# Kernel tuning notes

Measured on AMD Instinct MI355X. Metric: run time of the kernel, lower is better.

Reference implementation:

```python
import jax, jax.numpy as jnp
import numpy as np

N_NODES = 50000
BN_EPS = 1e-5


def setup_inputs() -> dict:
    key = jax.random.key(0)
    ks = jax.random.split(key, 16)
    N, IN, H, OUT, E = N_NODES, 512, 128, 64, 800000
    s = lambda fi, fo: 1.0 / np.sqrt(fi)
    inp = {
        'x': jax.random.normal(ks[0], (N, IN), dtype=jnp.float32),
        'edge_index': jax.random.randint(ks[1], (2, E), 0, N, dtype=jnp.int32),
        # mlpA: Linear(N -> H)
        'WA': jax.random.uniform(ks[2], (H, N), jnp.float32, -s(N, H), s(N, H)),
        'bA': jax.random.uniform(ks[3], (H,), jnp.float32, -s(N, H), s(N, H)),
        # mlpX: Linear(IN -> H)
        'WX': jax.random.uniform(ks[4], (H, IN), jnp.float32, -s(IN, H), s(IN, H)),
        'bX': jax.random.uniform(ks[5], (H,), jnp.float32, -s(IN, H), s(IN, H)),
        # W: Linear(2H -> H)
        'W': jax.random.uniform(ks[6], (H, 2 * H), jnp.float32, -s(2 * H, H), s(2 * H, H)),
        'bW': jax.random.uniform(ks[7], (H,), jnp.float32, -s(2 * H, H), s(2 * H, H)),
        # mlp_final layer 1: Linear(H -> H) + BN
        'Wf1': jax.random.uniform(ks[8], (H, H), jnp.float32, -s(H, H), s(H, H)),
        'bf1': jax.random.uniform(ks[9], (H,), jnp.float32, -s(H, H), s(H, H)),
        'gamma': jnp.ones((H,), jnp.float32),
        'beta': jnp.zeros((H,), jnp.float32),
        # mlp_final layer 2: Linear(H -> OUT)
        'Wf2': jax.random.uniform(ks[10], (OUT, H), jnp.float32, -s(H, OUT), s(H, OUT)),
        'bf2': jax.random.uniform(ks[11], (OUT,), jnp.float32, -s(H, OUT), s(H, OUT)),
    }
    return inp


def _batchnorm(x, gamma, beta):
    # training-mode BN over the node/batch axis (biased variance, as in torch)
    mean = jnp.mean(x, axis=0)
    var = jnp.var(x, axis=0)
    return (x - mean) * jax.lax.rsqrt(var + BN_EPS) * gamma + beta


def reference(x, edge_index, WA, bA, WX, bX, W, bW, Wf1, bf1, gamma, beta, Wf2, bf2):
    row, col = edge_index[0], edge_index[1]
    row = row - row.min()
    # xA = A @ WA.T + bA  where A[i,j]=1 per (row,col) edge (duplicates sum).
    # Equivalent SpMM: gather columns of WA at `col`, segment-sum into `row`.
    xA = jax.ops.segment_sum(WA.T[col], row, num_segments=N_NODES) + bA  # [N, H]
    xX = x @ WX.T + bX  # [N, H]
    h = jnp.concatenate([xA, xX], axis=-1) @ W.T + bW  # [N, H]
    h = jax.nn.relu(h + xA + xX)
    # mlp_final (num_layers=2): Linear -> ReLU -> BN -> (dropout off) -> Linear
    h = jax.nn.relu(h @ Wf1.T + bf1)
    h = _batchnorm(h, gamma, beta)
    out = h @ Wf2.T + bf2  # [N, OUT]
    return out
```

## Files before the change

### kernel.cpp

```cpp
#include <hip/hip_runtime.h>

typedef __bf16 bf16_t;
typedef __bf16 bf16x8 __attribute__((ext_vector_type(8)));
typedef float f32x4 __attribute__((ext_vector_type(4)));

#define IN_DIM 512
#define H_DIM 128
#define OUT_DIM 64
#define BN_EPS 1e-5f
#define SCAN_BLK 2048

#define MFMA(a, b, c) __builtin_amdgcn_mfma_f32_16x16x32_bf16(a, b, c, 0, 0, 0)

__device__ __forceinline__ float ld_adapt(const void* p, size_t i, int isbf) {
    return isbf ? (float)((const bf16_t*)p)[i] : ((const float*)p)[i];
}

__device__ __forceinline__ void split8(const float* p, bf16x8& hi, bf16x8& lo) {
    f32x4 v0 = *(const f32x4*)p;
    f32x4 v1 = *(const f32x4*)(p + 4);
#pragma unroll
    for (int i = 0; i < 8; ++i) {
        float f = (i < 4) ? v0[i] : v1[i - 4];
        bf16_t h = (bf16_t)f;
        hi[i] = h;
        lo[i] = (bf16_t)(f - (float)h);
    }
}

__global__ void k_init(const void* bA, const void* bX, const void* bW, const void* bf1,
                       const void* gamma, const void* beta, const void* bf2,
                       float* __restrict__ dst, int* __restrict__ flag) {
    __shared__ int s_isbf;
    if (threadIdx.x == 0) {
        unsigned u = *(const unsigned*)gamma;
        int f = (u == 0x3F803F80u) ? 1 : 0;
        *flag = f;
        s_isbf = f;
    }
    __syncthreads();
    int isbf = s_isbf;
    int t = threadIdx.x;
    dst[t] = ld_adapt(bA, t, isbf);
    dst[128 + t] = ld_adapt(bX, t, isbf);
    dst[256 + t] = ld_adapt(bW, t, isbf);
    dst[384 + t] = ld_adapt(bf1, t, isbf);
    dst[512 + t] = ld_adapt(gamma, t, isbf);
    dst[640 + t] = ld_adapt(beta, t, isbf);
    if (t < OUT_DIM) dst[768 + t] = ld_adapt(bf2, t, isbf);
}

__global__ __launch_bounds__(256) void k_transpose(const void* __restrict__ WA,
                                                   float* __restrict__ WAT, int N,
                                                   const int* __restrict__ flag) {
    __shared__ float t[64][130];
    int isbf = *flag;
    int n0 = blockIdx.x * 64;
    int tid = threadIdx.x;
#pragma unroll
    for (int i = 0; i < 32; ++i) {
        int lin = i * 256 + tid;
        int h = lin >> 6, nl = lin & 63;
        int n = n0 + nl;
        t[nl][h] = (n < N) ? ld_adapt(WA, (size_t)h * N + n, isbf) : 0.f;
    }
    __syncthreads();
#pragma unroll
    for (int i = 0; i < 32; ++i) {
        int lin = i * 256 + tid;
        int nl = lin >> 7, h = lin & 127;
        int n = n0 + nl;
        if (n < N) WAT[(size_t)n * H_DIM + h] = t[nl][h];
    }
}

__global__ __launch_bounds__(256) void k_prep(const int* __restrict__ rows, int E,
                                              int* __restrict__ bmin, int* __restrict__ cnt) {
    __shared__ int sm[4];
    int i = blockIdx.x * 256 + threadIdx.x;
    int m = 0x7fffffff;
    if (i < E) {
        int r = rows[i];
        m = r;
        atomicAdd(&cnt[r], 1);
    }
    for (int off = 32; off; off >>= 1) m = min(m, __shfl_xor(m, off, 64));
    if ((threadIdx.x & 63) == 0) sm[threadIdx.x >> 6] = m;
    __syncthreads();
    if (threadIdx.x == 0)
        bmin[blockIdx.x] = min(min(sm[0], sm[1]), min(sm[2], sm[3]));
}

__global__ __launch_bounds__(256) void k_scan1(const int* __restrict__ cnt,
                                               int* __restrict__ offs,
                                               int* __restrict__ bsum, int N) {
    __shared__ int ts[256];
    int base = blockIdx.x * SCAN_BLK;
    int t = threadIdx.x;
    int v[8], s = 0;
#pragma unroll
    for (int i = 0; i < 8; ++i) {
        int idx = base + t * 8 + i;
        v[i] = (idx < N) ? cnt[idx] : 0;
        s += v[i];
    }
    ts[t] = s;
    __syncthreads();
    for (int off = 1; off < 256; off <<= 1) {
        int x = (t >= off) ? ts[t - off] : 0;
        __syncthreads();
        ts[t] += x;
        __syncthreads();
    }
    int run = ts[t] - s;
#pragma unroll
    for (int i = 0; i < 8; ++i) {
        int idx = base + t * 8 + i;
        if (idx < N) offs[idx] = run;
        run += v[i];
    }
    if (t == 255) bsum[blockIdx.x] = ts[255];
}

__global__ __launch_bounds__(256) void k_scan2(int* __restrict__ bsum, int* __restrict__ offs,
                                               int NB, int N, const int* __restrict__ bmin,
                                               int nbmin, int* __restrict__ minbuf) {
    __shared__ int sm[256];
    int t = threadIdx.x;
    int m = 0x7fffffff;
    for (int i = t; i < nbmin; i += 256) m = min(m, bmin[i]);
    sm[t] = m;
    __syncthreads();
    for (int off = 128; off; off >>= 1) {
        if (t < off) sm[t] = min(sm[t], sm[t + off]);
        __syncthreads();
    }
    if (t == 0) {
        *minbuf = sm[0];
        int run = 0;
        for (int b = 0; b < NB; ++b) {
            int v = bsum[b];
            bsum[b] = run;
            run += v;
        }
        offs[N] = run;
    }
}

__global__ __launch_bounds__(256) void k_scan3(int* __restrict__ offs, const int* __restrict__ bsum,
                                               int* __restrict__ cursor, int N) {
    int i = blockIdx.x * 256 + threadIdx.x;
    if (i >= N) return;
    int v = offs[i] + bsum[i / SCAN_BLK];
    offs[i] = v;
    cursor[i] = v;
}

__global__ __launch_bounds__(256) void k_build(const int* __restrict__ rows,
                                               const int* __restrict__ cols, int E,
                                               int* __restrict__ cursor,
                                               int* __restrict__ scol) {
    int i = blockIdx.x * 256 + threadIdx.x;
    if (i >= E) return;
    int r = rows[i];
    int pos = atomicAdd(&cursor[r], 1);
    scol[pos] = cols[i];
}

__global__ __launch_bounds__(256) void k_gather(const int* __restrict__ offs,
                                                const int* __restrict__ scol,
                                                const float* __restrict__ WAT,
                                                const float* __restrict__ bA_f,
                                                const int* __restrict__ minbuf,
                                                float* __restrict__ xA, int N) {
    int wave = threadIdx.x >> 6, lane = threadIdx.x & 63;
    int r = blockIdx.x * 4 + wave;
    if (r >= N) return;
    int b = r + *minbuf;
    int s = 0, e = 0;
    if (b < N) {
        s = offs[b];
        e = offs[b + 1];
    }
    float2 a0 = {0.f, 0.f}, a1 = {0.f, 0.f};
    int i = s;
    for (; i + 3 < e; i += 4) {
        int c0 = scol[i], c1 = scol[i + 1], c2 = scol[i + 2], c3 = scol[i + 3];
        float2 w0 = *(const float2*)(WAT + (size_t)c0 * H_DIM + lane * 2);
        float2 w1 = *(const float2*)(WAT + (size_t)c1 * H_DIM + lane * 2);
        float2 w2 = *(const float2*)(WAT + (size_t)c2 * H_DIM + lane * 2);
        float2 w3 = *(const float2*)(WAT + (size_t)c3 * H_DIM + lane * 2);
        a0.x += w0.x + w2.x; a0.y += w0.y + w2.y;
        a1.x += w1.x + w3.x; a1.y += w1.y + w3.y;
    }
    for (; i < e; ++i) {
        int c = scol[i];
        float2 w = *(const float2*)(WAT + (size_t)c * H_DIM + lane * 2);
        a0.x += w.x; a0.y += w.y;
    }
    float2 bias = *(const float2*)(bA_f + lane * 2);
    float2 out = {a0.x + a1.x + bias.x, a0.y + a1.y + bias.y};
    *(float2*)(xA + (size_t)r * H_DIM + lane * 2) = out;
}

__device__ __forceinline__ void pack_frag(const void* __restrict__ W, bf16_t* __restrict__ hi,
                                          bf16_t* __restrict__ lo, int K, int NC,
                                          int addres, int isbf, int f, int lane) {
    int ks = f / (NC >> 4), nt = f % (NC >> 4);
    int n = nt * 16 + (lane & 15);
    int k0 = ks * 32 + (lane >> 4) * 8;
    bf16_t* dh = hi + (size_t)f * 512 + lane * 8;
    bf16_t* dl = lo + (size_t)f * 512 + lane * 8;
#pragma unroll
    for (int j = 0; j < 8; ++j) {
        int kk = k0 + j;
        float v = ld_adapt(W, (size_t)n * K + kk, isbf);
        if (addres && (kk == n || kk == n + H_DIM)) v += 1.f;
        bf16_t h = (bf16_t)v;
        dh[j] = h;
        dl[j] = (bf16_t)(v - (float)h);
    }
}

__global__ __launch_bounds__(256) void k_pack3(const void* WX, bf16_t* WXh, bf16_t* WXl,
                                               const void* W, bf16_t* Wh, bf16_t* Wl,
                                               const void* Wf1, bf16_t* Wf1h, bf16_t* Wf1l,
                                               const int* __restrict__ flag) {
    int g = blockIdx.x * 256 + threadIdx.x;
    int f = g >> 6, lane = g & 63;
    int isbf = *flag;
    if (f < 128)
        pack_frag(WX, WXh, WXl, IN_DIM, H_DIM, 0, isbf, f, lane);
    else if (f < 192)
        pack_frag(W, Wh, Wl, 2 * H_DIM, H_DIM, 1, isbf, f - 128, lane);
    else if (f < 224)
        pack_frag(Wf1, Wf1h, Wf1l, H_DIM, H_DIM, 0, isbf, f - 192, lane);
}

__global__ __launch_bounds__(512) void k_fuseA(
    const void* __restrict__ x, const float* __restrict__ xAf,
    const bf16_t* __restrict__ WXh, const bf16_t* __restrict__ WXl,
    const bf16_t* __restrict__ Wh, const bf16_t* __restrict__ Wl,
    const bf16_t* __restrict__ Wf1h, const bf16_t* __restrict__ Wf1l,
    const float* __restrict__ smallf, float* __restrict__ h2,
    double* __restrict__ sums, double* __restrict__ sumsq,
    const int* __restrict__ flag, int M) {
    __shared__ float ax[64 * 132];
    __shared__ float ls_sum[H_DIM], ls_sq[H_DIM];
    int tid = threadIdx.x;
    int wave = tid >> 6, lane = tid & 63, l16 = lane & 15, quad = lane >> 4;
    int band = wave & 3, half = wave >> 2;
    int ntb = half * 4;
    int mbase = blockIdx.x * 64 + band * 16;
    int isbf = *flag;
    int r0 = min(mbase + l16, M - 1);
    const float* bX = smallf + 128;
    const float* bW = smallf + 256;
    const float* bf1 = smallf + 384;

    if (tid < H_DIM) {
        ls_sum[tid] = 0.f;
        ls_sq[tid] = 0.f;
    }

    bf16x8 zero8;
#pragma unroll
    for (int i = 0; i < 8; ++i) zero8[i] = (bf16_t)0.f;

    f32x4 acc[4];
#pragma unroll
    for (int nt = 0; nt < 4; ++nt) acc[nt] = f32x4{0.f, 0.f, 0.f, 0.f};
    {
        size_t offx = (size_t)r0 * IN_DIM + quad * 8;
        for (int ks = 0; ks < 16; ++ks) {
            bf16x8 ah, al;
            if (isbf) {
                ah = *(const bf16x8*)((const bf16_t*)x + offx + ks * 32);
                al = zero8;
            } else {
                split8((const float*)x + offx + ks * 32, ah, al);
            }
            const bf16_t* bhp = WXh + ((size_t)ks * 8 + ntb) * 512 + lane * 8;
            const bf16_t* blp = WXl + ((size_t)ks * 8 + ntb) * 512 + lane * 8;
#pragma unroll
            for (int nt = 0; nt < 4; ++nt) {
                bf16x8 bh = *(const bf16x8*)(bhp + nt * 512);
                bf16x8 bl = *(const bf16x8*)(blp + nt * 512);
                acc[nt] = MFMA(ah, bh, acc[nt]);
                acc[nt] = MFMA(ah, bl, acc[nt]);
                acc[nt] = MFMA(al, bh, acc[nt]);
            }
        }
    }
#pragma unroll
    for (int nt = 0; nt < 4; ++nt) {
        int col = (ntb + nt) * 16 + l16;
        float b = bX[col];
#pragma unroll
        for (int r = 0; r < 4; ++r) {
            int lr = band * 16 + quad * 4 + r;
            ax[lr * 132 + col] = acc[nt][r] + b;
        }
    }
    __syncthreads();

#pragma unroll
    for (int nt = 0; nt < 4; ++nt) acc[nt] = f32x4{0.f, 0.f, 0.f, 0.f};
    for (int ks = 0; ks < 8; ++ks) {
        bf16x8 ah, al;
        if (ks < 4)
            split8(xAf + (size_t)r0 * H_DIM + ks * 32 + quad * 8, ah, al);
        else
            split8(ax + (band * 16 + l16) * 132 + (ks - 4) * 32 + quad * 8, ah, al);
        const bf16_t* bhp = Wh + ((size_t)ks * 8 + ntb) * 512 + lane * 8;
        const bf16_t* blp = Wl + ((size_t)ks * 8 + ntb) * 512 + lane * 8;
#pragma unroll
        for (int nt = 0; nt < 4; ++nt) {
            bf16x8 bh = *(const bf16x8*)(bhp + nt * 512);
            bf16x8 bl = *(const bf16x8*)(blp + nt * 512);
            acc[nt] = MFMA(ah, bh, acc[nt]);
            acc[nt] = MFMA(ah, bl, acc[nt]);
            acc[nt] = MFMA(al, bh, acc[nt]);
        }
    }
    __syncthreads();
#pragma unroll
    for (int nt = 0; nt < 4; ++nt) {
        int col = (ntb + nt) * 16 + l16;
        float b = bW[col];
#pragma unroll
        for (int r = 0; r < 4; ++r) {
            int lr = band * 16 + quad * 4 + r;
            ax[lr * 132 + col] = fmaxf(acc[nt][r] + b, 0.f);
        }
    }
    __syncthreads();

#pragma unroll
    for (int nt = 0; nt < 4; ++nt) acc[nt] = f32x4{0.f, 0.f, 0.f, 0.f};
    for (int ks = 0; ks < 4; ++ks) {
        bf16x8 ah, al;
        split8(ax + (band * 16 + l16) * 132 + ks * 32 + quad * 8, ah, al);
        const bf16_t* bhp = Wf1h + ((size_t)ks * 8 + ntb) * 512 + lane * 8;
        const bf16_t* blp = Wf1l + ((size_t)ks * 8 + ntb) * 512 + lane * 8;
#pragma unroll
        for (int nt = 0; nt < 4; ++nt) {
            bf16x8 bh = *(const bf16x8*)(bhp + nt * 512);
            bf16x8 bl = *(const bf16x8*)(blp + nt * 512);
            acc[nt] = MFMA(ah, bh, acc[nt]);
            acc[nt] = MFMA(ah, bl, acc[nt]);
            acc[nt] = MFMA(al, bh, acc[nt]);
        }
    }
#pragma unroll
    for (int nt = 0; nt < 4; ++nt) {
        int col = (ntb + nt) * 16 + l16;
        float b = bf1[col];
        float s = 0.f, s2 = 0.f;
#pragma unroll
        for (int r = 0; r < 4; ++r) {
            int row = mbase + quad * 4 + r;
            if (row < M) {
                float v = fmaxf(acc[nt][r] + b, 0.f);
                h2[(size_t)row * H_DIM + col] = v;
                s += v;
                s2 += v * v;
            }
        }
        s += __shfl_xor(s, 16, 64);
        s += __shfl_xor(s, 32, 64);
        s2 += __shfl_xor(s2, 16, 64);
        s2 += __shfl_xor(s2, 32, 64);
        if (quad == 0) {
            atomicAdd(&ls_sum[col], s);
            atomicAdd(&ls_sq[col], s2);
        }
    }
    __syncthreads();
    if (tid < H_DIM) {
        atomicAdd(&sums[tid], (double)ls_sum[tid]);
        atomicAdd(&sumsq[tid], (double)ls_sq[tid]);
    }
}

__global__ __launch_bounds__(256) void k_fuseB(
    const float* __restrict__ h2, const void* __restrict__ Wf2,
    const float* __restrict__ smallf, const double* __restrict__ sums,
    const double* __restrict__ sumsq, void* __restrict__ outv,
    const int* __restrict__ flag, int M) {
    __shared__ bf16_t wh[16 * 512];
    __shared__ bf16_t wl[16 * 512];
    __shared__ float aw[H_DIM], cw[H_DIM], b2[OUT_DIM];
    int t = threadIdx.x;
    int isbf = *flag;
    const float* gamma_f = smallf + 512;
    const float* beta_f = smallf + 640;
    const float* bf2_f = smallf + 768;

    if (t < H_DIM) {
        double mean = sums[t] / (double)M;
        double var = sumsq[t] / (double)M - mean * mean;
        if (var < 0) var = 0;
        float a = gamma_f[t] * rsqrtf((float)var + BN_EPS);
        aw[t] = a;
        cw[t] = beta_f[t] - (float)mean * a;
    }
    __syncthreads();
    if (t < OUT_DIM) {
        float acc = bf2_f[t];
        for (int j = 0; j < H_DIM; ++j) acc += ld_adapt(Wf2, (size_t)t * H_DIM + j, isbf) * cw[j];
        b2[t] = acc;
    }
    for (int u = t; u < 1024; u += 256) {
        int f = u >> 6, ln = u & 63;
        int ks = f >> 2, nt = f & 3;
        int n = nt * 16 + (ln & 15);
        int k0 = ks * 32 + (ln >> 4) * 8;
#pragma unroll
        for (int j = 0; j < 8; ++j) {
            float v = ld_adapt(Wf2, (size_t)n * H_DIM + k0 + j, isbf) * aw[k0 + j];
            bf16_t h = (bf16_t)v;
            wh[f * 512 + ln * 8 + j] = h;
            wl[f * 512 + ln * 8 + j] = (bf16_t)(v - (float)h);
        }
    }
    __syncthreads();

    int wave = t >> 6, lane = t & 63, l16 = lane & 15, quad = lane >> 4;
    int mbase = blockIdx.x * 64 + wave * 16;
    int r0 = min(mbase + l16, M - 1);
    f32x4 acc4[4];
#pragma unroll
    for (int nt = 0; nt < 4; ++nt) acc4[nt] = f32x4{0.f, 0.f, 0.f, 0.f};
    for (int ks = 0; ks < 4; ++ks) {
        bf16x8 ah, al;
        split8(h2 + (size_t)r0 * H_DIM + ks * 32 + quad * 8, ah, al);
#pragma unroll
        for (int nt = 0; nt < 4; ++nt) {
            bf16x8 bh = *(const bf16x8*)(wh + (ks * 4 + nt) * 512 + lane * 8);
            bf16x8 bl = *(const bf16x8*)(wl + (ks * 4 + nt) * 512 + lane * 8);
            acc4[nt] = MFMA(ah, bh, acc4[nt]);
            acc4[nt] = MFMA(ah, bl, acc4[nt]);
            acc4[nt] = MFMA(al, bh, acc4[nt]);
        }
    }
#pragma unroll
    for (int nt = 0; nt < 4; ++nt) {
        int col = nt * 16 + l16;
        float b = b2[col];
#pragma unroll
        for (int r = 0; r < 4; ++r) {
            int row = mbase + quad * 4 + r;
            if (row < M) {
                float v = acc4[nt][r] + b;
                if (isbf)
                    ((bf16_t*)outv)[(size_t)row * OUT_DIM + col] = (bf16_t)v;
                else
                    ((float*)outv)[(size_t)row * OUT_DIM + col] = v;
            }
        }
    }
}

extern "C" void kernel_launch(void* const* d_in, const int* in_sizes, int n_in,
                              void* d_out, int out_size, void* d_ws, size_t ws_size,
                              hipStream_t stream) {
    const void* x = d_in[0];
    const int* ei = (const int*)d_in[1];
    const void* WA = d_in[2];
    const void* bA = d_in[3];
    const void* WX = d_in[4];
    const void* bX = d_in[5];
    const void* W = d_in[6];
    const void* bW = d_in[7];
    const void* Wf1 = d_in[8];
    const void* bf1 = d_in[9];
    const void* gamma = d_in[10];
    const void* beta = d_in[11];
    const void* Wf2 = d_in[12];
    const void* bf2 = d_in[13];

    const int N = in_sizes[0] / IN_DIM;
    const int E = in_sizes[1] / 2;
    const int* rows = ei;
    const int* cols = ei + E;
    const int eblocks = (E + 255) / 256;

    char* ws = (char*)d_ws;
    size_t off = 0;
    auto alloc = [&](size_t bytes) {
        char* p = ws + off;
        off += (bytes + 255) & ~(size_t)255;
        return p;
    };
    int* flag = (int*)alloc(4);
    int* minbuf = (int*)alloc(4);
    float* smallf = (float*)alloc(832 * 4);
    double* sums = (double*)alloc(2 * H_DIM * 8);
    double* sumsq = sums + H_DIM;
    bf16_t* WXp_h = (bf16_t*)alloc((size_t)IN_DIM * H_DIM * 2);
    bf16_t* WXp_l = (bf16_t*)alloc((size_t)IN_DIM * H_DIM * 2);
    bf16_t* Wp_h = (bf16_t*)alloc((size_t)256 * H_DIM * 2);
    bf16_t* Wp_l = (bf16_t*)alloc((size_t)256 * H_DIM * 2);
    bf16_t* Wf1p_h = (bf16_t*)alloc((size_t)H_DIM * H_DIM * 2);
    bf16_t* Wf1p_l = (bf16_t*)alloc((size_t)H_DIM * H_DIM * 2);
    int* cnt = (int*)alloc((size_t)N * 4);
    int* offs = (int*)alloc(((size_t)N + 1) * 4);
    int* cursor = (int*)alloc((size_t)N * 4);
    int* bsum = (int*)alloc(64 * 4);
    int* bmin = (int*)alloc((size_t)eblocks * 4);
    int* scol = (int*)alloc((size_t)E * 4);
    float* WAT = (float*)alloc((size_t)N * H_DIM * 4);
    float* xAf = (float*)alloc((size_t)N * H_DIM * 4);
    float* h2 = WAT;

    float* bA_f = smallf + 0;

    hipMemsetAsync(cnt, 0, (size_t)N * 4, stream);
    hipMemsetAsync(sums, 0, 2 * H_DIM * 8, stream);

    k_init<<<1, 128, 0, stream>>>(bA, bX, bW, bf1, gamma, beta, bf2, smallf, flag);
    k_transpose<<<(N + 63) / 64, 256, 0, stream>>>(WA, WAT, N, flag);
    k_pack3<<<56, 256, 0, stream>>>(WX, WXp_h, WXp_l, W, Wp_h, Wp_l, Wf1, Wf1p_h, Wf1p_l, flag);

    k_prep<<<eblocks, 256, 0, stream>>>(rows, E, bmin, cnt);
    int NB = (N + SCAN_BLK - 1) / SCAN_BLK;
    k_scan1<<<NB, 256, 0, stream>>>(cnt, offs, bsum, N);
    k_scan2<<<1, 256, 0, stream>>>(bsum, offs, NB, N, bmin, eblocks, minbuf);
    k_scan3<<<(N + 255) / 256, 256, 0, stream>>>(offs, bsum, cursor, N);
    k_build<<<eblocks, 256, 0, stream>>>(rows, cols, E, cursor, scol);
    k_gather<<<(N + 3) / 4, 256, 0, stream>>>(offs, scol, WAT, bA_f, minbuf, xAf, N);

    int fblocks = (N + 63) / 64;
    k_fuseA<<<fblocks, 512, 0, stream>>>(x, xAf, WXp_h, WXp_l, Wp_h, Wp_l, Wf1p_h, Wf1p_l,
                                         smallf, h2, sums, sumsq, flag, N);
    k_fuseB<<<fblocks, 256, 0, stream>>>(h2, Wf2, smallf, sums, sumsq, d_out, flag, N);
}
```

Measured before the change: 487.7 us.

## Software-pipeline fused MLP loads, shrink blocks, and widen gather unroll

The fused MLP kernel now double-buffers its A and B operand loads from global memory, so the next k-step's data is fetched while the current MFMAs run. Blocks shrink from 64 rows and 512 threads to 32 rows and 256 threads, with launch bounds asking for two blocks per CU. The SpMM gather loop is unrolled to 8 loads with four accumulators to keep more memory requests in flight. The extra prefetch buffers raise register pressure, which could reduce occupancy.

Measured after the change: 503.5 us. 1.03x slower.

```diff
diff --git a/kernel.cpp b/kernel.cpp
--- a/kernel.cpp
+++ b/kernel.cpp
@@ -25,6 +25,34 @@
         bf16_t h = (bf16_t)f;
         hi[i] = h;
         lo[i] = (bf16_t)(f - (float)h);
+    }
+}
+
+__device__ __forceinline__ void loadAraw(const void* x, size_t elemoff, int isbf,
+                                         f32x4& p0, f32x4& p1) {
+    if (isbf) {
+        p0 = *(const f32x4*)((const bf16_t*)x + elemoff);
+    } else {
+        const float* fp = (const float*)x + elemoff;
+        p0 = *(const f32x4*)fp;
+        p1 = *(const f32x4*)(fp + 4);
+    }
+}
+
+__device__ __forceinline__ void cvtA(const f32x4& p0, const f32x4& p1, int isbf,
+                                     bf16x8& ah, bf16x8& al) {
+    if (isbf) {
+        ah = __builtin_bit_cast(bf16x8, p0);
+#pragma unroll
+        for (int i = 0; i < 8; ++i) al[i] = (bf16_t)0.f;
+    } else {
+#pragma unroll
+        for (int i = 0; i < 8; ++i) {
+            float f = (i < 4) ? p0[i] : p1[i - 4];
+            bf16_t h = (bf16_t)f;
+            ah[i] = h;
+            al[i] = (bf16_t)(f - (float)h);
+        }
     }
 }
 
@@ -182,24 +210,34 @@
         s = offs[b];
         e = offs[b + 1];
     }
-    float2 a0 = {0.f, 0.f}, a1 = {0.f, 0.f};
+    float2 a0 = {0.f, 0.f}, a1 = {0.f, 0.f}, a2 = {0.f, 0.f}, a3 = {0.f, 0.f};
     int i = s;
-    for (; i + 3 < e; i += 4) {
-        int c0 = scol[i], c1 = scol[i + 1], c2 = scol[i + 2], c3 = scol[i + 3];
+    for (; i + 7 < e; i += 8) {
+        float2 w[8];
+#pragma unroll
+        for (int j = 0; j < 8; ++j) {
+            int c = scol[i + j];
+            w[j] = *(const float2*)(WAT + (size_t)c * H_DIM + lane * 2);
+        }
+        a0.x += w[0].x + w[4].x; a0.y += w[0].y + w[4].y;
+        a1.x += w[1].x + w[5].x; a1.y += w[1].y + w[5].y;
+        a2.x += w[2].x + w[6].x; a2.y += w[2].y + w[6].y;
+        a3.x += w[3].x + w[7].x; a3.y += w[3].y + w[7].y;
+    }
+    for (; i + 1 < e; i += 2) {
+        int c0 = scol[i], c1 = scol[i + 1];
         float2 w0 = *(const float2*)(WAT + (size_t)c0 * H_DIM + lane * 2);
         float2 w1 = *(const float2*)(WAT + (size_t)c1 * H_DIM + lane * 2);
-        float2 w2 = *(const float2*)(WAT + (size_t)c2 * H_DIM + lane * 2);
-        float2 w3 = *(const float2*)(WAT + (size_t)c3 * H_DIM + lane * 2);
-        a0.x += w0.x + w2.x; a0.y += w0.y + w2.y;
-        a1.x += w1.x + w3.x; a1.y += w1.y + w3.y;
-    }
-    for (; i < e; ++i) {
+        a0.x += w0.x; a0.y += w0.y;
+        a1.x += w1.x; a1.y += w1.y;
+    }
+    if (i < e) {
         int c = scol[i];
         float2 w = *(const float2*)(WAT + (size_t)c * H_DIM + lane * 2);
-        a0.x += w.x; a0.y += w.y;
+        a2.x += w.x; a2.y += w.y;
     }
     float2 bias = *(const float2*)(bA_f + lane * 2);
-    float2 out = {a0.x + a1.x + bias.x, a0.y + a1.y + bias.y};
+    float2 out = {a0.x + a1.x + a2.x + a3.x + bias.x, a0.y + a1.y + a2.y + a3.y + bias.y};
     *(float2*)(xA + (size_t)r * H_DIM + lane * 2) = out;
 }
 
@@ -237,7 +275,7 @@
         pack_frag(Wf1, Wf1h, Wf1l, H_DIM, H_DIM, 0, isbf, f - 192, lane);
 }
 
-__global__ __launch_bounds__(512) void k_fuseA(
+__global__ __launch_bounds__(256, 2) void k_fuseA(
     const void* __restrict__ x, const float* __restrict__ xAf,
     const bf16_t* __restrict__ WXh, const bf16_t* __restrict__ WXl,
     const bf16_t* __restrict__ Wh, const bf16_t* __restrict__ Wl,
@@ -245,13 +283,13 @@
     const float* __restrict__ smallf, float* __restrict__ h2,
     double* __restrict__ sums, double* __restrict__ sumsq,
     const int* __restrict__ flag, int M) {
-    __shared__ float ax[64 * 132];
+    __shared__ float ax[32 * 132];
     __shared__ float ls_sum[H_DIM], ls_sq[H_DIM];
     int tid = threadIdx.x;
     int wave = tid >> 6, lane = tid & 63, l16 = lane & 15, quad = lane >> 4;
-    int band = wave & 3, half = wave >> 2;
+    int band = wave & 1, half = wave >> 1;
     int ntb = half * 4;
-    int mbase = blockIdx.x * 64 + band * 16;
+    int mbase = blockIdx.x * 32 + band * 16;
     int isbf = *flag;
     int r0 = min(mbase + l16, M - 1);
     const float* bX = smallf + 128;
@@ -263,32 +301,41 @@
         ls_sq[tid] = 0.f;
     }
 
-    bf16x8 zero8;
-#pragma unroll
-    for (int i = 0; i < 8; ++i) zero8[i] = (bf16_t)0.f;
+    auto loadB = [&](const bf16_t* __restrict__ H, const bf16_t* __restrict__ L, int fb,
+                     bf16x8 bh[4], bf16x8 bl[4]) {
+        const bf16_t* hp = H + (size_t)fb * 512 + lane * 8;
+        const bf16_t* lp = L + (size_t)fb * 512 + lane * 8;
+#pragma unroll
+        for (int nt = 0; nt < 4; ++nt) {
+            bh[nt] = *(const bf16x8*)(hp + nt * 512);
+            bl[nt] = *(const bf16x8*)(lp + nt * 512);
+        }
+    };
 
     f32x4 acc[4];
+    bf16x8 bh[2][4], bl[2][4];
+    f32x4 pa[2][2];
+
 #pragma unroll
     for (int nt = 0; nt < 4; ++nt) acc[nt] = f32x4{0.f, 0.f, 0.f, 0.f};
     {
         size_t offx = (size_t)r0 * IN_DIM + quad * 8;
+        loadAraw(x, offx, isbf, pa[0][0], pa[0][1]);
+        loadB(WXh, WXl, ntb, bh[0], bl[0]);
+#pragma unroll
         for (int ks = 0; ks < 16; ++ks) {
+            int cur = ks & 1, nxt = cur ^ 1;
+            if (ks < 15) {
+                loadAraw(x, offx + (ks + 1) * 32, isbf, pa[nxt][0], pa[nxt][1]);
+                loadB(WXh, WXl, (ks + 1) * 8 + ntb, bh[nxt], bl[nxt]);
+            }
             bf16x8 ah, al;
-            if (isbf) {
-                ah = *(const bf16x8*)((const bf16_t*)x + offx + ks * 32);
-                al = zero8;
-            } else {
-                split8((const float*)x + offx + ks * 32, ah, al);
-            }
-            const bf16_t* bhp = WXh + ((size_t)ks * 8 + ntb) * 512 + lane * 8;
-            const bf16_t* blp = WXl + ((size_t)ks * 8 + ntb) * 512 + lane * 8;
+            cvtA(pa[cur][0], pa[cur][1], isbf, ah, al);
 #pragma unroll
             for (int nt = 0; nt < 4; ++nt) {
-                bf16x8 bh = *(const bf16x8*)(bhp + nt * 512);
-                bf16x8 bl = *(const bf16x8*)(blp + nt * 512);
-                acc[nt] = MFMA(ah, bh, acc[nt]);
-                acc[nt] = MFMA(ah, bl, acc[nt]);
-                acc[nt] = MFMA(al, bh, acc[nt]);
+                acc[nt] = MFMA(ah, bh[cur][nt], acc[nt]);
+                acc[nt] = MFMA(ah, bl[cur][nt], acc[nt]);
+                acc[nt] = MFMA(al, bh[cur][nt], acc[nt]);
             }
         }
     }
@@ -306,21 +353,31 @@
 
 #pragma unroll
     for (int nt = 0; nt < 4; ++nt) acc[nt] = f32x4{0.f, 0.f, 0.f, 0.f};
-    for (int ks = 0; ks < 8; ++ks) {
-        bf16x8 ah, al;
-        if (ks < 4)
-            split8(xAf + (size_t)r0 * H_DIM + ks * 32 + quad * 8, ah, al);
-        else
-            split8(ax + (band * 16 + l16) * 132 + (ks - 4) * 32 + quad * 8, ah, al);
-        const bf16_t* bhp = Wh + ((size_t)ks * 8 + ntb) * 512 + lane * 8;
-        const bf16_t* blp = Wl + ((size_t)ks * 8 + ntb) * 512 + lane * 8;
-#pragma unroll
-        for (int nt = 0; nt < 4; ++nt) {
-            bf16x8 bh = *(const bf16x8*)(bhp + nt * 512);
-            bf16x8 bl = *(const bf16x8*)(blp + nt * 512);
-            acc[nt] = MFMA(ah, bh, acc[nt]);
-            acc[nt] = MFMA(ah, bl, acc[nt]);
-            acc[nt] = MFMA(al, bh, acc[nt]);
+    {
+        size_t aoff = (size_t)r0 * H_DIM + quad * 8;
+        const float* axp = ax + (band * 16 + l16) * 132 + quad * 8;
+        pa[0][0] = *(const f32x4*)(xAf + aoff);
+        pa[0][1] = *(const f32x4*)(xAf + aoff + 4);
+        loadB(Wh, Wl, ntb, bh[0], bl[0]);
+#pragma unroll
+        for (int ks = 0; ks < 8; ++ks) {
+            int cur = ks & 1, nxt = cur ^ 1;
+            if (ks < 7) loadB(Wh, Wl, (ks + 1) * 8 + ntb, bh[nxt], bl[nxt]);
+            if (ks < 3) {
+                pa[nxt][0] = *(const f32x4*)(xAf + aoff + (ks + 1) * 32);
+                pa[nxt][1] = *(const f32x4*)(xAf + aoff + (ks + 1) * 32 + 4);
+            }
+            bf16x8 ah, al;
+            if (ks < 4)
+                cvtA(pa[cur][0], pa[cur][1], 0, ah, al);
+            else
+                split8(axp + (ks - 4) * 32, ah, al);
+#pragma unroll
+            for (int nt = 0; nt < 4; ++nt) {
+                acc[nt] = MFMA(ah, bh[cur][nt], acc[nt]);
+                acc[nt] = MFMA(ah, bl[cur][nt], acc[nt]);
+                acc[nt] = MFMA(al, bh[cur][nt], acc[nt]);
+            }
         }
     }
     __syncthreads();
@@ -338,18 +395,21 @@
 
 #pragma unroll
     for (int nt = 0; nt < 4; ++nt) acc[nt] = f32x4{0.f, 0.f, 0.f, 0.f};
-    for (int ks = 0; ks < 4; ++ks) {
-        bf16x8 ah, al;
-        split8(ax + (band * 16 + l16) * 132 + ks * 32 + quad * 8, ah, al);
-        const bf16_t* bhp = Wf1h + ((size_t)ks * 8 + ntb) * 512 + lane * 8;
-        const bf16_t* blp = Wf1l + ((size_t)ks * 8 + ntb) * 512 + lane * 8;
-#pragma unroll
-        for (int nt = 0; nt < 4; ++nt) {
-            bf16x8 bh = *(const bf16x8*)(bhp + nt * 512);
-            bf16x8 bl = *(const bf16x8*)(blp + nt * 512);
-            acc[nt] = MFMA(ah, bh, acc[nt]);
-            acc[nt] = MFMA(ah, bl, acc[nt]);
-            acc[nt] = MFMA(al, bh, acc[nt]);
+    {
+        const float* axp = ax + (band * 16 + l16) * 132 + quad * 8;
+        loadB(Wf1h, Wf1l, ntb, bh[0], bl[0]);
+#pragma unroll
+        for (int ks = 0; ks < 4; ++ks) {
+            int cur = ks & 1, nxt = cur ^ 1;
+            if (ks < 3) loadB(Wf1h, Wf1l, (ks + 1) * 8 + ntb, bh[nxt], bl[nxt]);
+            bf16x8 ah, al;
+            split8(axp + ks * 32, ah, al);
+#pragma unroll
+            for (int nt = 0; nt < 4; ++nt) {
+                acc[nt] = MFMA(ah, bh[cur][nt], acc[nt]);
+                acc[nt] = MFMA(ah, bl[cur][nt], acc[nt]);
+                acc[nt] = MFMA(al, bh[cur][nt], acc[nt]);
+            }
         }
     }
 #pragma unroll
@@ -531,8 +591,7 @@
     k_build<<<eblocks, 256, 0, stream>>>(rows, cols, E, cursor, scol);
     k_gather<<<(N + 3) / 4, 256, 0, stream>>>(offs, scol, WAT, bA_f, minbuf, xAf, N);
 
-    int fblocks = (N + 63) / 64;
-    k_fuseA<<<fblocks, 512, 0, stream>>>(x, xAf, WXp_h, WXp_l, Wp_h, Wp_l, Wf1p_h, Wf1p_l,
-                                         smallf, h2, sums, sumsq, flag, N);
-    k_fuseB<<<fblocks, 256, 0, stream>>>(h2, Wf2, smallf, sums, sumsq, d_out, flag, N);
-}
+    k_fuseA<<<(N + 31) / 32, 256, 0, stream>>>(x, xAf, WXp_h, WXp_l, Wp_h, Wp_l, Wf1p_h, Wf1p_l,
+                                               smallf, h2, sums, sumsq, flag, N);
+    k_fuseB<<<(N + 63) / 64, 256, 0, stream>>>(h2, Wf2, smallf, sums, sumsq, d_out, flag, N);
+}
```
